# Performance work log

Hardware: AMD Instinct MI355X
Metric: run time of the kernel (lower is better)

## Reference

```python
import jax, jax.numpy as jnp
import numpy as np

B, C, H, W = 2, 64, 96, 96
DQK = C // 8  # query/key channel dim = 8


def setup_inputs() -> dict:
    key = jax.random.key(0)
    ks = jax.random.split(key, 8)
    s = 0.05
    x = jax.random.normal(ks[0], (B, C, H, W), dtype=jnp.float32)
    Wq = jax.random.normal(ks[1], (DQK, C), dtype=jnp.float32) * s
    bq = jax.random.normal(ks[2], (DQK,), dtype=jnp.float32) * s
    Wk = jax.random.normal(ks[3], (DQK, C), dtype=jnp.float32) * s
    bk = jax.random.normal(ks[4], (DQK,), dtype=jnp.float32) * s
    Wv = jax.random.normal(ks[5], (C, C), dtype=jnp.float32) * s
    bv = jax.random.normal(ks[6], (C,), dtype=jnp.float32) * s
    gamma = jax.random.normal(ks[7], (1,), dtype=jnp.float32) * s
    return {"x": x, "Wq": Wq, "bq": bq, "Wk": Wk, "bk": bk,
            "Wv": Wv, "bv": bv, "gamma": gamma}


def _attend(x, Wq, bq, Wk, bk, Wv, bv, gamma):
    b, c, h, w = x.shape
    p = h * w
    xf = x.reshape(b, c, p)                                    # [B,C,P]
    # 1x1 convs == per-pixel linear maps
    q = jnp.einsum('dc,bcp->bpd', Wq, xf) + bq                 # [B,P,d]
    k = jnp.einsum('dc,bcp->bdp', Wk, xf) + bk[None, :, None]  # [B,d,P]
    v = jnp.einsum('oc,bcp->bop', Wv, xf) + bv[None, :, None]  # [B,C,P]
    # energy[b,i,j] = q_i . k_j ; softmax over keys j (no 1/sqrt(d) scale,
    # matching the original module)
    energy = jnp.einsum('bpd,bdq->bpq', q, k)                  # [B,P,P]
    attn = jax.nn.softmax(energy, axis=-1)                     # [B,P,P]
    out = jnp.einsum('bcq,bpq->bcp', v, attn)                  # [B,C,P]
    out = out.reshape(b, c, h, w)
    return gamma * out + x


def reference(x, Wq, bq, Wk, bk, Wv, bv, gamma):
    return _attend(x, Wq, bq, Wk, bk, Wv, bv, gamma)
```

## Files before the change

kernel.cpp:

```cpp
#include <hip/hip_runtime.h>
#include <hip/hip_bf16.h>
#include <stdint.h>

#define BB 2
#define CC 64
#define PP 9216
#define QTILES 144
#define LOG2E 1.4426950408889634f
#define SCH_C 16248.664965f
#define SCH_BC 12599160.0f

typedef unsigned short ushort;
typedef __attribute__((ext_vector_type(8))) short short8;
typedef __attribute__((ext_vector_type(4))) float floatx4;
typedef __attribute__((ext_vector_type(4))) int intx4;

__device__ __forceinline__ ushort f2bf(float f) {
    unsigned int u = __float_as_uint(f);
    u = (u + 0x7fffu + ((u >> 16) & 1u)) >> 16;
    return (ushort)u;
}

__device__ __forceinline__ unsigned int exp2_pk_bf16(float e0, float e1) {
    const float t0 = fmaf(e0, 128.f, SCH_BC);
    const float t1 = fmaf(e1, 128.f, SCH_BC);
    return __builtin_amdgcn_perm(__float_as_uint(t1), __float_as_uint(t0),
                                 0x05040100u);
}

__global__ __launch_bounds__(256)
void proj3(const float* __restrict__ x,
           const float* __restrict__ Wq, const float* __restrict__ bq,
           const float* __restrict__ Wk, const float* __restrict__ bk,
           const float* __restrict__ Wv, const float* __restrict__ bv,
           ushort* __restrict__ qbuf, ushort* __restrict__ kbuf,
           ushort* __restrict__ vfw)
{
    const int tid = threadIdx.x;
    const int px  = tid & 63;
    const int og  = __builtin_amdgcn_readfirstlane(tid >> 6);
    const int blk = blockIdx.x;
    const int b     = blk / (2 * QTILES);
    const int rem   = blk % (2 * QTILES);
    const int ptile = rem >> 1;
    const int rhalf = rem & 1;
    const int p     = ptile * 64 + px;
    const int r0    = rhalf * 40 + og * 10;

    const float* wr[10];
#pragma unroll
    for (int r = 0; r < 10; ++r) {
        const int row = r0 + r;
        wr[r] = (row < 8) ? (Wq + row * 64)
              : (row < 16) ? (Wk + (row - 8) * 64)
              : (Wv + (row - 16) * 64);
    }

    float xv[64];
#pragma unroll
    for (int c = 0; c < 64; ++c)
        xv[c] = x[((size_t)b * 64 + c) * PP + p];

    float acc[10];
#pragma unroll
    for (int r = 0; r < 10; ++r) acc[r] = 0.f;
#pragma unroll
    for (int c = 0; c < 64; ++c) {
#pragma unroll
        for (int r = 0; r < 10; ++r)
            acc[r] = fmaf(wr[r][c], xv[c], acc[r]);
    }

#pragma unroll
    for (int r = 0; r < 10; ++r) {
        const int row = r0 + r;
        if (row < 8) {
            const float v = (acc[r] + bq[row]) * LOG2E;
            qbuf[((size_t)b * PP + p) * 8 + row] = f2bf(v);
        } else if (row < 16) {
            const float v = acc[r] + bk[row - 8];
            kbuf[((size_t)b * PP + p) * 8 + (row - 8)] = f2bf(v);
        } else {
            const int co = row - 16;
            const float v = acc[r] + bv[co];
            const int pl = p & 31;
            const int ps = (p & ~31) | ((((pl >> 2) & 3) << 3) | (((pl >> 4) & 1) << 2) | (pl & 3));
            vfw[((size_t)b * 64 + co) * PP + ps] = f2bf(v);
        }
    }
}

__global__ __launch_bounds__(128, 3)
void attn8(const ushort* __restrict__ qbuf, const ushort* __restrict__ kbuf,
           const ushort* __restrict__ vfw,
           ushort* __restrict__ accp, float* __restrict__ lsump,
           int keysPerG, int numTiles)
{
    __shared__ __align__(16) float smerge[64 * 64];
    __shared__ float slsum[64];

    const int tid  = threadIdx.x;
    const int lane = tid & 63;
    const int wid  = tid >> 6;
    const int col  = lane & 15;
    const int quad = lane >> 4;

    const int qt = blockIdx.x % QTILES;
    const int gb = blockIdx.x / QTILES;
    const int b  = gb % BB;
    const int g  = gb / BB;
    const int q0 = qt * 64;

    const short8 zf = {0, 0, 0, 0, 0, 0, 0, 0};
    const short vone = (short)0x3F80;
    const short8 vones = {vone, vone, vone, vone, vone, vone, vone, vone};

    short8 qfragB[4];
#pragma unroll
    for (int qh = 0; qh < 4; ++qh)
        qfragB[qh] = (quad == 0)
            ? *(const short8*)(qbuf + ((size_t)b * PP + q0 + qh * 16 + col) * 8)
            : zf;

    floatx4 acc[4][4];
#pragma unroll
    for (int qh = 0; qh < 4; ++qh)
#pragma unroll
        for (int cb = 0; cb < 4; ++cb) acc[qh][cb] = (floatx4){0.f, 0.f, 0.f, 0.f};
    floatx4 accLh[4];
#pragma unroll
    for (int qh = 0; qh < 4; ++qh) accLh[qh] = (floatx4){0.f, 0.f, 0.f, 0.f};

    const ushort* kB = kbuf + (size_t)b * PP * 8;
    const ushort* vB = vfw + (size_t)b * 64 * PP;
    const int kwbase = g * keysPerG + wid * 32;

    auto tile_load = [&](int t, short8& kf0, short8& kf1, short8 (&vf)[4]) {
        const int kw = kwbase + t * 64;
        kf0 = *(const short8*)(kB + (size_t)(kw + col) * 8 + quad * 8);
        kf1 = *(const short8*)(kB + (size_t)(kw + 16 + col) * 8 + quad * 8);
#pragma unroll
        for (int cb = 0; cb < 4; ++cb)
            vf[cb] = *(const short8*)(vB + ((size_t)(cb * 16 + col)) * PP + kw + quad * 8);
    };

    auto tile_compute = [&](const short8& kf0, const short8& kf1,
                            const short8 (&vf)[4]) {
#pragma unroll
        for (int qh = 0; qh < 4; ++qh) {
            const floatx4 E0 = __builtin_amdgcn_mfma_f32_16x16x32_bf16(
                kf0, qfragB[qh], (floatx4){0.f, 0.f, 0.f, 0.f}, 0, 0, 0);
            const floatx4 E1 = __builtin_amdgcn_mfma_f32_16x16x32_bf16(
                kf1, qfragB[qh], (floatx4){0.f, 0.f, 0.f, 0.f}, 0, 0, 0);

            intx4 pi;
            pi.x = (int)exp2_pk_bf16(E0[0], E0[1]);
            pi.y = (int)exp2_pk_bf16(E0[2], E0[3]);
            pi.z = (int)exp2_pk_bf16(E1[0], E1[1]);
            pi.w = (int)exp2_pk_bf16(E1[2], E1[3]);
            const short8 pf = __builtin_bit_cast(short8, pi);

            accLh[qh] = __builtin_amdgcn_mfma_f32_16x16x32_bf16(vones, pf, accLh[qh], 0, 0, 0);
#pragma unroll
            for (int cb = 0; cb < 4; ++cb)
                acc[qh][cb] = __builtin_amdgcn_mfma_f32_16x16x32_bf16(
                    vf[cb], pf, acc[qh][cb], 0, 0, 0);
        }
    };

    short8 kf0A, kf1A, vfA[4];
    short8 kf0B, kf1B, vfB[4];
    tile_load(0, kf0A, kf1A, vfA);

    for (int t = 0; t < numTiles; t += 2) {
        tile_load(t + 1, kf0B, kf1B, vfB);
        tile_compute(kf0A, kf1A, vfA);
        const int t2 = (t + 2 < numTiles) ? (t + 2) : (t + 1);
        tile_load(t2, kf0A, kf1A, vfA);
        tile_compute(kf0B, kf1B, vfB);
    }

    if (wid == 1) {
#pragma unroll
        for (int qh = 0; qh < 4; ++qh)
#pragma unroll
            for (int cb = 0; cb < 4; ++cb)
#pragma unroll
                for (int r = 0; r < 4; ++r)
                    smerge[(cb * 16 + quad * 4 + r) * 64 + qh * 16 + col] = acc[qh][cb][r];
        if (quad == 0)
#pragma unroll
            for (int qh = 0; qh < 4; ++qh)
                slsum[qh * 16 + col] = accLh[qh][0];
    }
    __syncthreads();
    if (wid == 0) {
        ushort* ab = accp + ((size_t)g * BB + b) * CC * PP;
#pragma unroll
        for (int qh = 0; qh < 4; ++qh)
#pragma unroll
            for (int cb = 0; cb < 4; ++cb)
#pragma unroll
                for (int r = 0; r < 4; ++r) {
                    const int c = cb * 16 + quad * 4 + r;
                    const float v = acc[qh][cb][r] + smerge[c * 64 + qh * 16 + col];
                    ab[(size_t)c * PP + q0 + qh * 16 + col] = f2bf(v);
                }
        if (quad == 0) {
            float* lb = lsump + ((size_t)g * BB + b) * PP + q0;
#pragma unroll
            for (int qh = 0; qh < 4; ++qh)
                lb[qh * 16 + col] = accLh[qh][0] + slsum[qh * 16 + col];
        }
    }
}

__global__ __launch_bounds__(256)
void combine(const ushort* __restrict__ accp, const float* __restrict__ lsump,
             const float* __restrict__ x, const float* __restrict__ gamma,
             float* __restrict__ out, int G)
{
    const size_t i8 = ((size_t)blockIdx.x * 256 + threadIdx.x) * 8;
    const int b = (int)(i8 / ((size_t)CC * PP));
    const int p = (int)(i8 % PP);
    const float gm = gamma[0];

    float asum[8] = {}, lst[8] = {};
    for (int g = 0; g < G; ++g) {
        const uint4 av = *(const uint4*)(accp + (size_t)g * (BB * CC * PP) + i8);
        const unsigned int u[4] = {av.x, av.y, av.z, av.w};
#pragma unroll
        for (int k = 0; k < 4; ++k) {
            asum[2 * k]     += __uint_as_float(u[k] << 16);
            asum[2 * k + 1] += __uint_as_float(u[k] & 0xffff0000u);
        }
        const float* lp = lsump + ((size_t)g * BB + b) * PP + p;
        const float4 l0 = *(const float4*)lp;
        const float4 l1 = *(const float4*)(lp + 4);
        lst[0] += l0.x; lst[1] += l0.y; lst[2] += l0.z; lst[3] += l0.w;
        lst[4] += l1.x; lst[5] += l1.y; lst[6] += l1.z; lst[7] += l1.w;
    }

    const float4 x0 = *(const float4*)(x + i8);
    const float4 x1 = *(const float4*)(x + i8 + 4);
    float o[8] = {x0.x, x0.y, x0.z, x0.w, x1.x, x1.y, x1.z, x1.w};
#pragma unroll
    for (int j = 0; j < 8; ++j)
        o[j] = fmaf(asum[j], gm / fmaxf(lst[j], 1e-30f), o[j]);
    *(float4*)(out + i8)     = make_float4(o[0], o[1], o[2], o[3]);
    *(float4*)(out + i8 + 4) = make_float4(o[4], o[5], o[6], o[7]);
}

extern "C" void kernel_launch(void* const* d_in, const int* in_sizes, int n_in,
                              void* d_out, int out_size, void* d_ws, size_t ws_size,
                              hipStream_t stream)
{
    const float* x     = (const float*)d_in[0];
    const float* Wq    = (const float*)d_in[1];
    const float* bq    = (const float*)d_in[2];
    const float* Wk    = (const float*)d_in[3];
    const float* bk    = (const float*)d_in[4];
    const float* Wv    = (const float*)d_in[5];
    const float* bv    = (const float*)d_in[6];
    const float* gamma = (const float*)d_in[7];
    float* out = (float*)d_out;

    const size_t nQK  = (size_t)BB * PP * 8;
    const size_t nV   = (size_t)BB * CC * PP;
    const size_t base = 2 * nQK * 2 + nV * 2;
    const size_t perG = nV * 2 + (size_t)BB * PP * 4;
    const int G = (ws_size >= base + 4 * perG) ? 4 : 2;
    const int keysPerG = PP / G;
    const int numTiles = keysPerG / 64;

    ushort* qbuf = (ushort*)d_ws;
    ushort* kbuf = qbuf + nQK;
    ushort* vfw  = kbuf + nQK;
    ushort* accp = vfw + nV;
    float* lsump = (float*)(accp + (size_t)G * nV);

    proj3<<<dim3(BB * 2 * QTILES), dim3(256), 0, stream>>>(
        x, Wq, bq, Wk, bk, Wv, bv, qbuf, kbuf, vfw);
    attn8<<<dim3(G * BB * QTILES), dim3(128), 0, stream>>>(
        qbuf, kbuf, vfw, accp, lsump, keysPerG, numTiles);
    combine<<<dim3(576), dim3(256), 0, stream>>>(
        accp, lsump, x, gamma, out, G);
}
```

Before: 140.1 us.

## Stage K/V tiles through LDS with async global_load_lds double buffering

Result: faster. 130.6 us (-6.8%).

```diff
diff --git a/kernel.cpp b/kernel.cpp
--- a/kernel.cpp
+++ b/kernel.cpp
@@ -7,7 +7,6 @@
 #define PP 9216
 #define QTILES 144
 #define LOG2E 1.4426950408889634f
-#define SCH_C 16248.664965f
 #define SCH_BC 12599160.0f
 
 typedef unsigned short ushort;
@@ -26,6 +25,12 @@
     const float t1 = fmaf(e1, 128.f, SCH_BC);
     return __builtin_amdgcn_perm(__float_as_uint(t1), __float_as_uint(t0),
                                  0x05040100u);
+}
+
+__device__ __forceinline__ void gload16_lds(const void* g, void* lds_base) {
+    __builtin_amdgcn_global_load_lds(
+        (const __attribute__((address_space(1))) unsigned int*)g,
+        (__attribute__((address_space(3))) unsigned int*)lds_base, 16, 0, 0);
 }
 
 __global__ __launch_bounds__(256)
@@ -91,17 +96,18 @@
 }
 
 __global__ __launch_bounds__(128, 3)
-void attn8(const ushort* __restrict__ qbuf, const ushort* __restrict__ kbuf,
-           const ushort* __restrict__ vfw,
-           ushort* __restrict__ accp, float* __restrict__ lsump,
-           int keysPerG, int numTiles)
+void attn10(const ushort* __restrict__ qbuf, const ushort* __restrict__ kbuf,
+            const ushort* __restrict__ vfw,
+            ushort* __restrict__ accp, float* __restrict__ lsump,
+            int keysPerG, int numTiles)
 {
-    __shared__ __align__(16) float smerge[64 * 64];
-    __shared__ float slsum[64];
+    __shared__ __align__(16) char sbuf[18688];
+    float* smerge = (float*)sbuf;
+    float* slsum  = (float*)(sbuf + 18432);
 
     const int tid  = threadIdx.x;
     const int lane = tid & 63;
-    const int wid  = tid >> 6;
+    const int kh   = tid >> 6;
     const int col  = lane & 15;
     const int quad = lane >> 4;
 
@@ -112,8 +118,6 @@
     const int q0 = qt * 64;
 
     const short8 zf = {0, 0, 0, 0, 0, 0, 0, 0};
-    const short vone = (short)0x3F80;
-    const short8 vones = {vone, vone, vone, vone, vone, vone, vone, vone};
 
     short8 qfragB[4];
 #pragma unroll
@@ -127,25 +131,39 @@
     for (int qh = 0; qh < 4; ++qh)
 #pragma unroll
         for (int cb = 0; cb < 4; ++cb) acc[qh][cb] = (floatx4){0.f, 0.f, 0.f, 0.f};
-    floatx4 accLh[4];
-#pragma unroll
-    for (int qh = 0; qh < 4; ++qh) accLh[qh] = (floatx4){0.f, 0.f, 0.f, 0.f};
+    float accL[4] = {0.f, 0.f, 0.f, 0.f};
 
     const ushort* kB = kbuf + (size_t)b * PP * 8;
     const ushort* vB = vfw + (size_t)b * 64 * PP;
-    const int kwbase = g * keysPerG + wid * 32;
-
-    auto tile_load = [&](int t, short8& kf0, short8& kf1, short8 (&vf)[4]) {
+    const int kwbase = g * keysPerG;
+
+    const int vr = lane >> 3;
+    const int vc = (lane & 7) ^ vr;
+
+    auto stage = [&](int t) {
         const int kw = kwbase + t * 64;
-        kf0 = *(const short8*)(kB + (size_t)(kw + col) * 8 + quad * 8);
-        kf1 = *(const short8*)(kB + (size_t)(kw + 16 + col) * 8 + quad * 8);
+        char* Vb = sbuf + (t & 1) * 9216;
+        if (kh == 0)
+            gload16_lds(kB + (size_t)(kw + lane) * 8, Vb + 8192);
+        const int j0 = kh * 4;
+#pragma unroll
+        for (int j = 0; j < 4; ++j) {
+            const int r = (j0 + j) * 8 + vr;
+            gload16_lds(vB + (size_t)r * PP + kw + vc * 8, Vb + (j0 + j) * 1024);
+        }
+    };
+
+    auto compute = [&](int t) {
+        const char* Vb = sbuf + (t & 1) * 9216;
+        const ushort* Kl = (const ushort*)(Vb + 8192);
+        const short8 kf0 = *(const short8*)(Kl + (kh * 32 + col) * 8);
+        const short8 kf1 = *(const short8*)(Kl + (kh * 32 + 16 + col) * 8);
+        short8 vf[4];
+        const int ce = (kh * 4 + quad) ^ (col & 7);
 #pragma unroll
         for (int cb = 0; cb < 4; ++cb)
-            vf[cb] = *(const short8*)(vB + ((size_t)(cb * 16 + col)) * PP + kw + quad * 8);
-    };
-
-    auto tile_compute = [&](const short8& kf0, const short8& kf1,
-                            const short8 (&vf)[4]) {
+            vf[cb] = *(const short8*)(Vb + ((cb * 16 + col) * 8 + ce) * 16);
+
 #pragma unroll
         for (int qh = 0; qh < 4; ++qh) {
             const floatx4 E0 = __builtin_amdgcn_mfma_f32_16x16x32_bf16(
@@ -160,7 +178,14 @@
             pi.w = (int)exp2_pk_bf16(E1[2], E1[3]);
             const short8 pf = __builtin_bit_cast(short8, pi);
 
-            accLh[qh] = __builtin_amdgcn_mfma_f32_16x16x32_bf16(vones, pf, accLh[qh], 0, 0, 0);
+            const unsigned int w0 = (unsigned int)pi.x, w1 = (unsigned int)pi.y;
+            const unsigned int w2 = (unsigned int)pi.z, w3 = (unsigned int)pi.w;
+            const float s0 = __uint_as_float(w0 << 16) + __uint_as_float(w0 & 0xffff0000u);
+            const float s1 = __uint_as_float(w1 << 16) + __uint_as_float(w1 & 0xffff0000u);
+            const float s2 = __uint_as_float(w2 << 16) + __uint_as_float(w2 & 0xffff0000u);
+            const float s3 = __uint_as_float(w3 << 16) + __uint_as_float(w3 & 0xffff0000u);
+            accL[qh] += (s0 + s1) + (s2 + s3);
+
 #pragma unroll
             for (int cb = 0; cb < 4; ++cb)
                 acc[qh][cb] = __builtin_amdgcn_mfma_f32_16x16x32_bf16(
@@ -168,19 +193,21 @@
         }
     };
 
-    short8 kf0A, kf1A, vfA[4];
-    short8 kf0B, kf1B, vfB[4];
-    tile_load(0, kf0A, kf1A, vfA);
-
-    for (int t = 0; t < numTiles; t += 2) {
-        tile_load(t + 1, kf0B, kf1B, vfB);
-        tile_compute(kf0A, kf1A, vfA);
-        const int t2 = (t + 2 < numTiles) ? (t + 2) : (t + 1);
-        tile_load(t2, kf0A, kf1A, vfA);
-        tile_compute(kf0B, kf1B, vfB);
-    }
-
-    if (wid == 1) {
+    stage(0);
+    __syncthreads();
+    for (int t = 0; t < numTiles; ++t) {
+        if (t + 1 < numTiles) stage(t + 1);
+        compute(t);
+        __syncthreads();
+    }
+
+#pragma unroll
+    for (int qh = 0; qh < 4; ++qh) {
+        accL[qh] += __shfl_xor(accL[qh], 16);
+        accL[qh] += __shfl_xor(accL[qh], 32);
+    }
+
+    if (kh == 1) {
 #pragma unroll
         for (int qh = 0; qh < 4; ++qh)
 #pragma unroll
@@ -191,10 +218,10 @@
         if (quad == 0)
 #pragma unroll
             for (int qh = 0; qh < 4; ++qh)
-                slsum[qh * 16 + col] = accLh[qh][0];
+                slsum[qh * 16 + col] = accL[qh];
     }
     __syncthreads();
-    if (wid == 0) {
+    if (kh == 0) {
         ushort* ab = accp + ((size_t)g * BB + b) * CC * PP;
 #pragma unroll
         for (int qh = 0; qh < 4; ++qh)
@@ -210,7 +237,7 @@
             float* lb = lsump + ((size_t)g * BB + b) * PP + q0;
 #pragma unroll
             for (int qh = 0; qh < 4; ++qh)
-                lb[qh * 16 + col] = accLh[qh][0] + slsum[qh * 16 + col];
+                lb[qh * 16 + col] = accL[qh] + slsum[qh * 16 + col];
         }
     }
 }
@@ -281,7 +308,7 @@
 
     proj3<<<dim3(BB * 2 * QTILES), dim3(256), 0, stream>>>(
         x, Wq, bq, Wk, bk, Wv, bv, qbuf, kbuf, vfw);
-    attn8<<<dim3(G * BB * QTILES), dim3(128), 0, stream>>>(
+    attn10<<<dim3(G * BB * QTILES), dim3(128), 0, stream>>>(
         qbuf, kbuf, vfw, accp, lsump, keysPerG, numTiles);
     combine<<<dim3(576), dim3(256), 0, stream>>>(
         accp, lsump, x, gamma, out, G);
```
